# Kernel tuning notes

Measured on AMD Instinct MI355X. Metric: run time of the kernel, lower is better.

The kernel has to match this reference:

```python
import jax, jax.numpy as jnp
import numpy as np

N = 100000      # nodes
E = 1600000     # edges (before self-loops)
IN = 128        # in_channels
H = 8           # heads (layer 0)
C = 8           # hidden_node_channels_per_head
OUT = 64        # out_channels (layer 1, single head, concat=False)
NEG_SLOPE = 0.2 # PyG GATConv LeakyReLU slope


def setup_inputs() -> dict:
    key = jax.random.key(0)
    ks = jax.random.split(key, 10)
    x = jax.random.normal(ks[0], (N, IN), jnp.float32)
    edge_index = jax.random.randint(ks[1], (2, E), 0, N, dtype=jnp.int32)
    s0 = 1.0 / np.sqrt(IN)
    s1 = 1.0 / np.sqrt(H * C)
    return {
        "x": x,
        "edge_index": edge_index,
        "W0": jax.random.normal(ks[2], (IN, H * C), jnp.float32) * s0,
        "att_src0": jax.random.normal(ks[3], (H, C), jnp.float32) * s1,
        "att_dst0": jax.random.normal(ks[4], (H, C), jnp.float32) * s1,
        "b0": jnp.zeros((H * C,), jnp.float32),
        "W1": jax.random.normal(ks[5], (H * C, OUT), jnp.float32) * s1,
        "att_src1": jax.random.normal(ks[6], (1, OUT), jnp.float32) * s1,
        "att_dst1": jax.random.normal(ks[7], (1, OUT), jnp.float32) * s1,
        "b1": jnp.zeros((OUT,), jnp.float32),
    }


def _gat_conv(x, src, dst, W, a_src, a_dst, b, heads, ch, concat):
    # x: [N, F_in]; src/dst: [E'] (self-loops included)
    xW = (x @ W).reshape(N, heads, ch)                     # [N, H, C]
    a_s = jnp.einsum('nhc,hc->nh', xW, a_src)              # [N, H]
    a_d = jnp.einsum('nhc,hc->nh', xW, a_dst)              # [N, H]
    e = jax.nn.leaky_relu(a_s[src] + a_d[dst], NEG_SLOPE)  # [E', H]
    # segment softmax over incoming edges of each dst node
    m = jax.ops.segment_max(e, dst, num_segments=N)        # [N, H]
    ex = jnp.exp(e - m[dst])
    denom = jax.ops.segment_sum(ex, dst, num_segments=N)   # [N, H]
    alpha = ex / denom[dst]                                # [E', H]
    out = jax.ops.segment_sum(alpha[:, :, None] * xW[src], dst, num_segments=N)  # [N, H, C]
    if concat:
        return out.reshape(N, heads * ch) + b
    return out.mean(axis=1) + b


def reference(x, edge_index, W0, att_src0, att_dst0, b0, W1, att_src1, att_dst1, b1):
    src, dst = edge_index[0], edge_index[1]
    loops = jnp.arange(N, dtype=src.dtype)                 # PyG add_self_loops=True
    src = jnp.concatenate([src, loops])
    dst = jnp.concatenate([dst, loops])
    # layer 0: GATConv(IN -> C per head, H heads, concat) ; ELU (dropout = identity at eval)
    h = jax.nn.elu(_gat_conv(x, src, dst, W0, att_src0, att_dst0, b0, H, C, True))
    # layer 1: GATConv(H*C -> OUT, 1 head, concat=False) ; ELU
    out = jax.nn.elu(_gat_conv(h, src, dst, W1, att_src1, att_dst1, b1, 1, OUT, False))
    return out
```

## Files before the change

### kernel.cpp

```cpp
#include <hip/hip_runtime.h>
#include <hip/hip_fp16.h>
#include <math.h>


#define CAPS 12
#define STRIDE 12
#define NBMAX 512
#define SLOTS 6144
#define OVF   1024
#define REGION 7168
#define LOG2E 1.44269504f

typedef _Float16 h2_t  __attribute__((ext_vector_type(2)));
typedef _Float16 h8_t  __attribute__((ext_vector_type(8)));
typedef float    f4_t  __attribute__((ext_vector_type(4)));
typedef unsigned int u4_t __attribute__((ext_vector_type(4)));

__device__ __forceinline__ float lrelu(float v) { return v >= 0.f ? v : 0.2f * v; }
__device__ __forceinline__ float eluf(float v)  {
    return v > 0.f ? v : __builtin_amdgcn_exp2f(v * LOG2E) - 1.f;
}

#define MIX_LO(acc, pk, w) asm("v_fma_mix_f32 %0, %1, %2, %0 op_sel:[0,0,0] op_sel_hi:[1,0,0]" : "+v"(acc) : "v"(pk), "v"(w))
#define MIX_HI(acc, pk, w) asm("v_fma_mix_f32 %0, %1, %2, %0 op_sel:[1,0,0] op_sel_hi:[1,0,0]" : "+v"(acc) : "v"(pk), "v"(w))

__device__ __forceinline__ void gemm_body(
    int gb, const float* __restrict__ x, int N,
    __half* __restrict__ xw, float* __restrict__ as, float* __restrict__ ad,
    h8_t* Bl)
{
    int wave = threadIdx.x >> 6, lane = threadIdx.x & 63;
    int row0 = gb * 128 + wave * 16;
    if (row0 >= N) return;
    int quad = lane >> 4, c16 = lane & 15;
    int myrow = min(row0 + c16, N - 1);
    const float* xr = x + (size_t)myrow * 128;
    h8_t a[4];
    #pragma unroll
    for (int ks = 0; ks < 4; ks++) {
        int kb = ks * 32 + quad * 8;
        float4 v0 = *(const float4*)(xr + kb);
        float4 v1 = *(const float4*)(xr + kb + 4);
        h8_t av;
        av[0] = (_Float16)v0.x; av[1] = (_Float16)v0.y;
        av[2] = (_Float16)v0.z; av[3] = (_Float16)v0.w;
        av[4] = (_Float16)v1.x; av[5] = (_Float16)v1.y;
        av[6] = (_Float16)v1.z; av[7] = (_Float16)v1.w;
        a[ks] = av;
    }
    int rbase = row0 + quad * 4;
    #pragma unroll
    for (int ct = 0; ct < 5; ct++) {
        f4_t acc = {0.f, 0.f, 0.f, 0.f};
        #pragma unroll
        for (int ks = 0; ks < 4; ks++) {
            h8_t b = Bl[(ct * 4 + ks) * 64 + lane];
            acc = __builtin_amdgcn_mfma_f32_16x16x32_f16(a[ks], b, acc, 0, 0, 0);
        }
        if (ct < 4) {
            int col = ct * 16 + c16;
            #pragma unroll
            for (int r = 0; r < 4; r++) {
                int row = rbase + r;
                if (row < N) xw[(size_t)row * 64 + col] = __float2half(acc[r]);
            }
        } else {
            #pragma unroll
            for (int r = 0; r < 4; r++) {
                int row = rbase + r;
                if (row < N) {
                    float sc = acc[r] * LOG2E;
                    if (c16 < 8) as[(size_t)row * 8 + c16] = sc;
                    else         ad[(size_t)row * 8 + (c16 - 8)] = sc;
                }
            }
        }
    }
}

__global__ __launch_bounds__(512, 4) void kGB(
    const float* __restrict__ x, const float* __restrict__ W0,
    const float* __restrict__ aS0, const float* __restrict__ aD0, int N,
    __half* __restrict__ xw, float* __restrict__ as, float* __restrict__ ad,
    int gemmBlocks,
    const int* __restrict__ src, const int* __restrict__ dst, int E, int perBlock,
    unsigned* __restrict__ bucketBuf, int* __restrict__ gcur, int* __restrict__ cntT,
    int NB, int binBlocks)
{
    __shared__ __align__(16) char smem[NBMAX * STRIDE * 4 + NBMAX * 4];
    int b = blockIdx.x;
    int T = gemmBlocks + binBlocks;
    int lo = (int)((long long)b * gemmBlocks / T);
    int hi = (int)((long long)(b + 1) * gemmBlocks / T);
    if (hi > lo) {
        h8_t* Bl = (h8_t*)smem;
        for (int g = threadIdx.x; g < 1280; g += 512) {
            int col  = g & 15;
            int quad = (g >> 4) & 3;
            int ks   = (g >> 6) & 3;
            int ct   = g >> 8;
            h8_t av;
            if (ct < 4) {
                #pragma unroll
                for (int j = 0; j < 8; j++) {
                    int k = ks * 32 + quad * 8 + j;
                    av[j] = (_Float16)W0[k * 64 + ct * 16 + col];
                }
            } else {
                int h = col & 7;
                const float* att = (col < 8) ? aS0 : aD0;
                #pragma unroll
                for (int j = 0; j < 8; j++) {
                    int k = ks * 32 + quad * 8 + j;
                    float v = 0.f;
                    #pragma unroll
                    for (int cc = 0; cc < 8; cc++)
                        v += W0[k * 64 + h * 8 + cc] * att[h * 8 + cc];
                    av[j] = (_Float16)v;
                }
            }
            Bl[g] = av;
        }
        __syncthreads();
        gemm_body(lo, x, N, xw, as, ad, Bl);
    } else {
        int pb = b - hi;
        unsigned* stage = (unsigned*)smem;
        int* scnt = (int*)(smem + NBMAX * STRIDE * 4);
        int tid = threadIdx.x;
        for (int i = tid; i < NB; i += 512) scnt[i] = 0;
        __syncthreads();
        int e0 = pb * perBlock, e1 = min(E, e0 + perBlock);
        for (int i = e0 + tid; i < e1; i += 512) {
            int d2 = dst[i], s2 = src[i];
            int bk = d2 >> 8;
            unsigned rec = ((unsigned)(d2 & 255) << 22) | (unsigned)s2;
            int pos = atomicAdd(&scnt[bk], 1);
            if (pos < CAPS) {
                stage[bk * STRIDE + pos] = rec;
            } else {
                int g = atomicAdd(&gcur[bk], 1);
                if (g < OVF) bucketBuf[(size_t)bk * REGION + SLOTS + g] = rec;
            }
        }
        __syncthreads();
        const uint4* stv = (const uint4*)stage;
        for (int t = tid; t < NB; t += 512) {
            int n = min(scnt[t], CAPS);
            cntT[(size_t)pb * NBMAX + t] = n;
            uint4* gp = (uint4*)&bucketBuf[(size_t)t * REGION + (size_t)pb * CAPS];
            gp[0] = stv[t * 3 + 0];
            gp[1] = stv[t * 3 + 1];
            gp[2] = stv[t * 3 + 2];
        }
    }
}

__global__ __launch_bounds__(256) void kP2(
    const unsigned* __restrict__ bucketBuf, const int* __restrict__ gcur,
    const int* __restrict__ cntT, int NB, int N,
    int* __restrict__ rowS, int* __restrict__ rowE, int* __restrict__ adj)
{
    __shared__ int cnts[512];
    __shared__ int deg[256];
    __shared__ int curl[256];
    __shared__ int sc[256];
    int b = blockIdx.x, tid = threadIdx.x;
    int lo = b << 8;
    int hi = min(N, lo + 256);
    int cnt = hi - lo;
    for (int i = tid; i < 512; i += 256) cnts[i] = cntT[(size_t)i * NBMAX + b];
    deg[tid] = 0;
    __syncthreads();
    const unsigned* buf = bucketBuf + (size_t)b * REGION;
    for (int blk = tid; blk < 512; blk += 256) {
        int c = cnts[blk];
        const unsigned* p = buf + blk * CAPS;
        for (int i2 = 0; i2 < c; i2++) atomicAdd(&deg[p[i2] >> 22], 1);
    }
    int ovf = min(gcur[b], OVF);
    for (int e = tid; e < ovf; e += 256) atomicAdd(&deg[buf[SLOTS + e] >> 22], 1);
    __syncthreads();
    int d = deg[tid];
    sc[tid] = d;
    __syncthreads();
    for (int off2 = 1; off2 < 256; off2 <<= 1) {
        int xv = (tid >= off2) ? sc[tid - off2] : 0;
        __syncthreads();
        sc[tid] += xv;
        __syncthreads();
    }
    int base = b * REGION;
    int o = (tid ? sc[tid - 1] : 0);
    curl[tid] = base + o;
    if (tid < cnt) { rowS[lo + tid] = base + o; rowE[lo + tid] = base + o + d; }
    __syncthreads();
    for (int blk = tid; blk < 512; blk += 256) {
        int c = cnts[blk];
        const unsigned* p = buf + blk * CAPS;
        for (int i2 = 0; i2 < c; i2++) {
            unsigned r = p[i2];
            int pp = atomicAdd(&curl[r >> 22], 1);
            adj[pp] = (int)(r & 0x3FFFFF);
        }
    }
    for (int e = tid; e < ovf; e += 256) {
        unsigned r = buf[SLOTS + e];
        int pp = atomicAdd(&curl[r >> 22], 1);
        adj[pp] = (int)(r & 0x3FFFFF);
    }
}

__global__ __launch_bounds__(512) void k_agg8(
    const __half* __restrict__ xw, const float* __restrict__ as, const float* __restrict__ ad,
    const int* __restrict__ rowS, const int* __restrict__ rowE, const int* __restrict__ adj,
    const float* __restrict__ bias,
    const float* __restrict__ W1, const float* __restrict__ aS1, const float* __restrict__ aD1,
    int N, __half* __restrict__ hw, float* __restrict__ as1, float* __restrict__ ad1)
{
    __shared__ __align__(16) h8_t Wl[512];
    __shared__ __align__(16) h8_t hst[32][9];
    {
        int g = threadIdx.x;
        int col  = g & 15;
        int quad = (g >> 4) & 3;
        int ks   = (g >> 6) & 1;
        int ct   = g >> 7;
        h8_t av;
        #pragma unroll
        for (int j = 0; j < 8; j++) {
            int k = ks * 32 + quad * 8 + j;
            av[j] = (_Float16)W1[k * 64 + ct * 16 + col];
        }
        Wl[g] = av;
    }
    int n = (blockIdx.x * 512 + threadIdx.x) >> 4;
    int sub  = threadIdx.x & 15;
    bool active = n < N;
    int e2 = sub >> 3;
    int hh = sub & 7;
    int rs = active ? rowS[n] : 0;
    int re = active ? rowE[n] : 0;
    const u4_t* xwv = (const u4_t*)xw;
    unsigned nc = active ? (unsigned)n : 0u;
    float adv = ad[nc * 8u + hh];
    float shift = lrelu(as[nc * 8u + hh] + adv);
    float accv[8];
    #pragma unroll
    for (int k = 0; k < 8; k++) accv[k] = 0.f;
    float dsum = 0.f;

    int j = rs;
    bool vA0 = j + e2 < re,     vB0 = j + 2 + e2 < re;
    int  sA0 = adj[(unsigned)(vA0 ? j + e2 : 0)];
    int  sB0 = adj[(unsigned)(vB0 ? j + 2 + e2 : 0)];
    bool vA1 = j + 4 + e2 < re, vB1 = j + 6 + e2 < re;
    int  sA1 = adj[(unsigned)(vA1 ? j + 4 + e2 : 0)];
    int  sB1 = adj[(unsigned)(vB1 ? j + 6 + e2 : 0)];
    float eA0 = lrelu(as[(unsigned)sA0 * 8u + hh] + adv);
    float eB0 = lrelu(as[(unsigned)sB0 * 8u + hh] + adv);
    u4_t xA0 = xwv[(unsigned)sA0 * 8u + hh];
    u4_t xB0 = xwv[(unsigned)sB0 * 8u + hh];
    float eA1, eB1; u4_t xA1, xB1;

    for (;;) {
        {
            bool vA2 = j + 8 + e2 < re, vB2 = j + 10 + e2 < re;
            int nsA = adj[(unsigned)(vA2 ? j + 8 + e2 : 0)];
            int nsB = adj[(unsigned)(vB2 ? j + 10 + e2 : 0)];
            eA1 = lrelu(as[(unsigned)sA1 * 8u + hh] + adv);
            eB1 = lrelu(as[(unsigned)sB1 * 8u + hh] + adv);
            xA1 = xwv[(unsigned)sA1 * 8u + hh];
            xB1 = xwv[(unsigned)sB1 * 8u + hh];
            float wA = vA0 ? __builtin_amdgcn_exp2f(eA0 - shift) : 0.f;
            float wB = vB0 ? __builtin_amdgcn_exp2f(eB0 - shift) : 0.f;
            dsum += wA + wB;
            #pragma unroll
            for (int q = 0; q < 4; q++) {
                MIX_LO(accv[2 * q],     xA0[q], wA);
                MIX_HI(accv[2 * q + 1], xA0[q], wA);
            }
            #pragma unroll
            for (int q = 0; q < 4; q++) {
                MIX_LO(accv[2 * q],     xB0[q], wB);
                MIX_HI(accv[2 * q + 1], xB0[q], wB);
            }
            vA0 = vA2; vB0 = vB2; sA0 = nsA; sB0 = nsB;
        }
        j += 4;
        if (!__any(vA1)) break;
        {
            bool vA2 = j + 8 + e2 < re, vB2 = j + 10 + e2 < re;
            int nsA = adj[(unsigned)(vA2 ? j + 8 + e2 : 0)];
            int nsB = adj[(unsigned)(vB2 ? j + 10 + e2 : 0)];
            eA0 = lrelu(as[(unsigned)sA0 * 8u + hh] + adv);
            eB0 = lrelu(as[(unsigned)sB0 * 8u + hh] + adv);
            xA0 = xwv[(unsigned)sA0 * 8u + hh];
            xB0 = xwv[(unsigned)sB0 * 8u + hh];
            float wA = vA1 ? __builtin_amdgcn_exp2f(eA1 - shift) : 0.f;
            float wB = vB1 ? __builtin_amdgcn_exp2f(eB1 - shift) : 0.f;
            dsum += wA + wB;
            #pragma unroll
            for (int q = 0; q < 4; q++) {
                MIX_LO(accv[2 * q],     xA1[q], wA);
                MIX_HI(accv[2 * q + 1], xA1[q], wA);
            }
            #pragma unroll
            for (int q = 0; q < 4; q++) {
                MIX_LO(accv[2 * q],     xB1[q], wB);
                MIX_HI(accv[2 * q + 1], xB1[q], wB);
            }
            vA1 = vA2; vB1 = vB2; sA1 = nsA; sB1 = nsB;
        }
        j += 4;
        if (!__any(vA0)) break;
    }
    #pragma unroll
    for (int k = 0; k < 8; k++) accv[k] += __shfl_xor(accv[k], 8, 64);
    dsum += __shfl_xor(dsum, 8, 64);
    if (e2 == 0) {
        int nl = (threadIdx.x >> 4);
        h8_t o;
        if (active) {
            float inv = 1.f / (1.f + dsum);
            h8_t sv = *(const h8_t*)(xw + (size_t)n * 64 + hh * 8);
            float4 b0 = *(const float4*)(bias + hh * 8);
            float4 b1 = *(const float4*)(bias + hh * 8 + 4);
            float bb[8] = {b0.x, b0.y, b0.z, b0.w, b1.x, b1.y, b1.z, b1.w};
            #pragma unroll
            for (int k = 0; k < 8; k++) {
                float v = (accv[k] + (float)sv[k]) * inv + bb[k];
                o[k] = (_Float16)eluf(v);
            }
        } else {
            #pragma unroll
            for (int k = 0; k < 8; k++) o[k] = (_Float16)0.f;
        }
        hst[nl][hh] = o;
    }
    __syncthreads();
    int wave = threadIdx.x >> 6, lane = threadIdx.x & 63;
    if (wave < 2) {
        int quad = lane >> 4, c16 = lane & 15;
        int lrow = wave * 16 + c16;
        int row0 = blockIdx.x * 32 + wave * 16;
        h8_t a0 = hst[lrow][quad];
        h8_t a1 = hst[lrow][4 + quad];
        int rbase = row0 + quad * 4;
        float ps[4] = {0.f, 0.f, 0.f, 0.f};
        float pd[4] = {0.f, 0.f, 0.f, 0.f};
        #pragma unroll
        for (int ct = 0; ct < 4; ct++) {
            f4_t acc = {0.f, 0.f, 0.f, 0.f};
            acc = __builtin_amdgcn_mfma_f32_16x16x32_f16(a0, Wl[(ct * 2 + 0) * 64 + lane], acc, 0, 0, 0);
            acc = __builtin_amdgcn_mfma_f32_16x16x32_f16(a1, Wl[(ct * 2 + 1) * 64 + lane], acc, 0, 0, 0);
            float s1c = aS1[ct * 16 + c16];
            float d1c = aD1[ct * 16 + c16];
            int col = ct * 16 + c16;
            #pragma unroll
            for (int r = 0; r < 4; r++) {
                int rr = rbase + r;
                if (rr < N) hw[(size_t)rr * 64 + col] = __float2half(acc[r]);
                ps[r] = fmaf(acc[r], s1c, ps[r]);
                pd[r] = fmaf(acc[r], d1c, pd[r]);
            }
        }
        #pragma unroll
        for (int r = 0; r < 4; r++) {
            #pragma unroll
            for (int off = 1; off < 16; off <<= 1) {
                ps[r] += __shfl_xor(ps[r], off, 64);
                pd[r] += __shfl_xor(pd[r], off, 64);
            }
        }
        if (c16 == 0) {
            #pragma unroll
            for (int r = 0; r < 4; r++) {
                int rr = rbase + r;
                if (rr < N) { as1[rr] = ps[r] * LOG2E; ad1[rr] = pd[r] * LOG2E; }
            }
        }
    }
}

__global__ __launch_bounds__(512) void k_agg1(
    const __half* __restrict__ hw, const float* __restrict__ as, const float* __restrict__ ad,
    const int* __restrict__ rowS, const int* __restrict__ rowE, const int* __restrict__ adj,
    const float* __restrict__ bias, int N, float* __restrict__ outp)
{
    int n = (blockIdx.x * 512 + threadIdx.x) >> 4;
    int sub  = threadIdx.x & 15;
    if (n >= N) return;
    int e2 = sub >> 3;
    int hh = sub & 7;
    int rs = rowS[n], re = rowE[n];
    const u4_t* hwv = (const u4_t*)hw;
    float adv = ad[n];
    float shift = lrelu(as[n] + adv);
    float accv[8];
    #pragma unroll
    for (int k = 0; k < 8; k++) accv[k] = 0.f;
    float dsum = 0.f;

    int j = rs;
    bool vA0 = j + e2 < re,     vB0 = j + 2 + e2 < re;
    int  sA0 = adj[(unsigned)(vA0 ? j + e2 : 0)];
    int  sB0 = adj[(unsigned)(vB0 ? j + 2 + e2 : 0)];
    bool vA1 = j + 4 + e2 < re, vB1 = j + 6 + e2 < re;
    int  sA1 = adj[(unsigned)(vA1 ? j + 4 + e2 : 0)];
    int  sB1 = adj[(unsigned)(vB1 ? j + 6 + e2 : 0)];
    float eA0 = lrelu(as[(unsigned)sA0] + adv);
    float eB0 = lrelu(as[(unsigned)sB0] + adv);
    u4_t xA0 = hwv[(unsigned)sA0 * 8u + hh];
    u4_t xB0 = hwv[(unsigned)sB0 * 8u + hh];
    float eA1, eB1; u4_t xA1, xB1;

    for (;;) {
        {
            bool vA2 = j + 8 + e2 < re, vB2 = j + 10 + e2 < re;
            int nsA = adj[(unsigned)(vA2 ? j + 8 + e2 : 0)];
            int nsB = adj[(unsigned)(vB2 ? j + 10 + e2 : 0)];
            eA1 = lrelu(as[(unsigned)sA1] + adv);
            eB1 = lrelu(as[(unsigned)sB1] + adv);
            xA1 = hwv[(unsigned)sA1 * 8u + hh];
            xB1 = hwv[(unsigned)sB1 * 8u + hh];
            float wA = vA0 ? __builtin_amdgcn_exp2f(eA0 - shift) : 0.f;
            float wB = vB0 ? __builtin_amdgcn_exp2f(eB0 - shift) : 0.f;
            dsum += wA + wB;
            #pragma unroll
            for (int q = 0; q < 4; q++) {
                MIX_LO(accv[2 * q],     xA0[q], wA);
                MIX_HI(accv[2 * q + 1], xA0[q], wA);
            }
            #pragma unroll
            for (int q = 0; q < 4; q++) {
                MIX_LO(accv[2 * q],     xB0[q], wB);
                MIX_HI(accv[2 * q + 1], xB0[q], wB);
            }
            vA0 = vA2; vB0 = vB2; sA0 = nsA; sB0 = nsB;
        }
        j += 4;
        if (!__any(vA1)) break;
        {
            bool vA2 = j + 8 + e2 < re, vB2 = j + 10 + e2 < re;
            int nsA = adj[(unsigned)(vA2 ? j + 8 + e2 : 0)];
            int nsB = adj[(unsigned)(vB2 ? j + 10 + e2 : 0)];
            eA0 = lrelu(as[(unsigned)sA0] + adv);
            eB0 = lrelu(as[(unsigned)sB0] + adv);
            xA0 = hwv[(unsigned)sA0 * 8u + hh];
            xB0 = hwv[(unsigned)sB0 * 8u + hh];
            float wA = vA1 ? __builtin_amdgcn_exp2f(eA1 - shift) : 0.f;
            float wB = vB1 ? __builtin_amdgcn_exp2f(eB1 - shift) : 0.f;
            dsum += wA + wB;
            #pragma unroll
            for (int q = 0; q < 4; q++) {
                MIX_LO(accv[2 * q],     xA1[q], wA);
                MIX_HI(accv[2 * q + 1], xA1[q], wA);
            }
            #pragma unroll
            for (int q = 0; q < 4; q++) {
                MIX_LO(accv[2 * q],     xB1[q], wB);
                MIX_HI(accv[2 * q + 1], xB1[q], wB);
            }
            vA1 = vA2; vB1 = vB2; sA1 = nsA; sB1 = nsB;
        }
        j += 4;
        if (!__any(vA0)) break;
    }
    #pragma unroll
    for (int k = 0; k < 8; k++) accv[k] += __shfl_xor(accv[k], 8, 64);
    dsum += __shfl_xor(dsum, 8, 64);
    if (e2 == 0) {
        float inv = 1.f / (1.f + dsum);
        h8_t sv = *(const h8_t*)(hw + (size_t)n * 64 + hh * 8);
        float4 b0 = *(const float4*)(bias + hh * 8);
        float4 b1 = *(const float4*)(bias + hh * 8 + 4);
        float bb[8] = {b0.x, b0.y, b0.z, b0.w, b1.x, b1.y, b1.z, b1.w};
        float ov[8];
        #pragma unroll
        for (int k = 0; k < 8; k++)
            ov[k] = eluf((accv[k] + (float)sv[k]) * inv + bb[k]);
        float4 o0 = {ov[0], ov[1], ov[2], ov[3]};
        float4 o1 = {ov[4], ov[5], ov[6], ov[7]};
        float4* op = (float4*)(outp + (size_t)n * 64 + hh * 8);
        op[0] = o0;
        op[1] = o1;
    }
}

extern "C" void kernel_launch(void* const* d_in, const int* in_sizes, int n_in,
                              void* d_out, int out_size, void* d_ws, size_t ws_size,
                              hipStream_t stream)
{
    const float* x   = (const float*)d_in[0];
    const int*   ei  = (const int*)d_in[1];
    const float* W0  = (const float*)d_in[2];
    const float* aS0 = (const float*)d_in[3];
    const float* aD0 = (const float*)d_in[4];
    const float* b0  = (const float*)d_in[5];
    const float* W1  = (const float*)d_in[6];
    const float* aS1 = (const float*)d_in[7];
    const float* aD1 = (const float*)d_in[8];
    const float* b1  = (const float*)d_in[9];

    const int N = in_sizes[0] / 128;
    const int E = in_sizes[1] / 2;
    const int* srcp = ei;
    const int* dstp = ei + E;

    const int NB  = (N + 255) >> 8;

    char* ws = (char*)d_ws;
    size_t off = 0;
    auto alloc = [&](size_t bytes) -> size_t {
        size_t o = off;
        off = (o + bytes + 255) & ~(size_t)255;
        return o;
    };
    __half* B1 = (__half*)(ws + alloc((size_t)N * 64 * 2));
    size_t b2Bytes = (size_t)N * 64 * 2;
    size_t bkBytes = (size_t)NB * REGION * 4;
    char*  region  = ws + alloc(b2Bytes > bkBytes ? b2Bytes : bkBytes);
    __half*   B2        = (__half*)region;
    unsigned* bucketBuf = (unsigned*)region;
    float* as0 = (float*)(ws + alloc((size_t)N * 8 * 4));
    float* ad0 = (float*)(ws + alloc((size_t)N * 8 * 4));
    float* as1 = (float*)(ws + alloc((size_t)N * 4));
    float* ad1 = (float*)(ws + alloc((size_t)N * 4));
    int*  rowS = (int*)(ws + alloc((size_t)(N + 1) * 4));
    int*  rowE = (int*)(ws + alloc((size_t)(N + 1) * 4));
    int*   adj = (int*)(ws + alloc((size_t)NB * REGION * 4));
    int*  gcur = (int*)(ws + alloc((size_t)NB * 4));
    int*  cntT = (int*)(ws + alloc((size_t)NBMAX * NBMAX * 4));

    const int gemmBlocks = (N + 127) / 128;
    const int binBlocks  = 512;
    const int perBlock   = (E + binBlocks - 1) / binBlocks;

    hipMemsetAsync(gcur, 0, (size_t)NB * 4, stream);
    kGB<<<gemmBlocks + binBlocks, 512, 0, stream>>>(
        x, W0, aS0, aD0, N, B1, as0, ad0, gemmBlocks,
        srcp, dstp, E, perBlock, bucketBuf, gcur, cntT, NB, binBlocks);
    kP2<<<NB, 256, 0, stream>>>(bucketBuf, gcur, cntT, NB, N, rowS, rowE, adj);

    const int agBlocks = (N + 31) / 32;
    k_agg8<<<agBlocks, 512, 0, stream>>>(B1, as0, ad0, rowS, rowE, adj, b0,
                                         W1, aS1, aD1, N, B2, as1, ad1);
    k_agg1<<<agBlocks, 512, 0, stream>>>(B2, as1, ad1, rowS, rowE, adj, b1, N, (float*)d_out);
}
```

Baseline: 238.5 us.

## Store layer-0 attention scores in fp16 and spread layer-1 GEMM across all waves

Layer-0 per-node attention logits (as0/ad0) are now written and gathered as fp16 instead of fp32, halving the bytes of the random per-edge gathers in the aggregation kernel. The fused layer-1 projection epilogue in k_agg8 is redistributed so all 8 waves each compute one column tile of one row half, instead of 2 waves looping over 4 column tiles. Partial attention dot products are then combined through shared memory with an extra barrier. The fp16 logits lower precision of the softmax inputs, and the epilogue change adds a sync and LDS traffic.

```diff
diff --git a/kernel.cpp b/kernel.cpp
--- a/kernel.cpp
+++ b/kernel.cpp
@@ -26,7 +26,7 @@
 
 __device__ __forceinline__ void gemm_body(
     int gb, const float* __restrict__ x, int N,
-    __half* __restrict__ xw, float* __restrict__ as, float* __restrict__ ad,
+    __half* __restrict__ xw, __half* __restrict__ as, __half* __restrict__ ad,
     h8_t* Bl)
 {
     int wave = threadIdx.x >> 6, lane = threadIdx.x & 63;
@@ -70,8 +70,8 @@
                 int row = rbase + r;
                 if (row < N) {
                     float sc = acc[r] * LOG2E;
-                    if (c16 < 8) as[(size_t)row * 8 + c16] = sc;
-                    else         ad[(size_t)row * 8 + (c16 - 8)] = sc;
+                    if (c16 < 8) as[(size_t)row * 8 + c16] = __float2half(sc);
+                    else         ad[(size_t)row * 8 + (c16 - 8)] = __float2half(sc);
                 }
             }
         }
@@ -81,7 +81,7 @@
 __global__ __launch_bounds__(512, 4) void kGB(
     const float* __restrict__ x, const float* __restrict__ W0,
     const float* __restrict__ aS0, const float* __restrict__ aD0, int N,
-    __half* __restrict__ xw, float* __restrict__ as, float* __restrict__ ad,
+    __half* __restrict__ xw, __half* __restrict__ as, __half* __restrict__ ad,
     int gemmBlocks,
     const int* __restrict__ src, const int* __restrict__ dst, int E, int perBlock,
     unsigned* __restrict__ bucketBuf, int* __restrict__ gcur, int* __restrict__ cntT,
@@ -212,7 +212,7 @@
 }
 
 __global__ __launch_bounds__(512) void k_agg8(
-    const __half* __restrict__ xw, const float* __restrict__ as, const float* __restrict__ ad,
+    const __half* __restrict__ xw, const __half* __restrict__ as, const __half* __restrict__ ad,
     const int* __restrict__ rowS, const int* __restrict__ rowE, const int* __restrict__ adj,
     const float* __restrict__ bias,
     const float* __restrict__ W1, const float* __restrict__ aS1, const float* __restrict__ aD1,
@@ -220,6 +220,8 @@
 {
     __shared__ __align__(16) h8_t Wl[512];
     __shared__ __align__(16) h8_t hst[32][9];
+    __shared__ float psum[4][32];
+    __shared__ float pdsum[4][32];
     {
         int g = threadIdx.x;
         int col  = g & 15;
@@ -243,8 +245,8 @@
     int re = active ? rowE[n] : 0;
     const u4_t* xwv = (const u4_t*)xw;
     unsigned nc = active ? (unsigned)n : 0u;
-    float adv = ad[nc * 8u + hh];
-    float shift = lrelu(as[nc * 8u + hh] + adv);
+    float adv = __half2float(ad[nc * 8u + hh]);
+    float shift = lrelu(__half2float(as[nc * 8u + hh]) + adv);
     float accv[8];
     #pragma unroll
     for (int k = 0; k < 8; k++) accv[k] = 0.f;
@@ -257,8 +259,8 @@
     bool vA1 = j + 4 + e2 < re, vB1 = j + 6 + e2 < re;
     int  sA1 = adj[(unsigned)(vA1 ? j + 4 + e2 : 0)];
     int  sB1 = adj[(unsigned)(vB1 ? j + 6 + e2 : 0)];
-    float eA0 = lrelu(as[(unsigned)sA0 * 8u + hh] + adv);
-    float eB0 = lrelu(as[(unsigned)sB0 * 8u + hh] + adv);
+    float eA0 = lrelu(__half2float(as[(unsigned)sA0 * 8u + hh]) + adv);
+    float eB0 = lrelu(__half2float(as[(unsigned)sB0 * 8u + hh]) + adv);
     u4_t xA0 = xwv[(unsigned)sA0 * 8u + hh];
     u4_t xB0 = xwv[(unsigned)sB0 * 8u + hh];
     float eA1, eB1; u4_t xA1, xB1;
@@ -268,8 +270,8 @@
             bool vA2 = j + 8 + e2 < re, vB2 = j + 10 + e2 < re;
             int nsA = adj[(unsigned)(vA2 ? j + 8 + e2 : 0)];
             int nsB = adj[(unsigned)(vB2 ? j + 10 + e2 : 0)];
-            eA1 = lrelu(as[(unsigned)sA1 * 8u + hh] + adv);
-            eB1 = lrelu(as[(unsigned)sB1 * 8u + hh] + adv);
+            eA1 = lrelu(__half2float(as[(unsigned)sA1 * 8u + hh]) + adv);
+            eB1 = lrelu(__half2float(as[(unsigned)sB1 * 8u + hh]) + adv);
             xA1 = xwv[(unsigned)sA1 * 8u + hh];
             xB1 = xwv[(unsigned)sB1 * 8u + hh];
             float wA = vA0 ? __builtin_amdgcn_exp2f(eA0 - shift) : 0.f;
@@ -293,8 +295,8 @@
             bool vA2 = j + 8 + e2 < re, vB2 = j + 10 + e2 < re;
             int nsA = adj[(unsigned)(vA2 ? j + 8 + e2 : 0)];
             int nsB = adj[(unsigned)(vB2 ? j + 10 + e2 : 0)];
-            eA0 = lrelu(as[(unsigned)sA0 * 8u + hh] + adv);
-            eB0 = lrelu(as[(unsigned)sB0 * 8u + hh] + adv);
+            eA0 = lrelu(__half2float(as[(unsigned)sA0 * 8u + hh]) + adv);
+            eB0 = lrelu(__half2float(as[(unsigned)sB0 * 8u + hh]) + adv);
             xA0 = xwv[(unsigned)sA0 * 8u + hh];
             xB0 = xwv[(unsigned)sB0 * 8u + hh];
             float wA = vA1 ? __builtin_amdgcn_exp2f(eA1 - shift) : 0.f;
@@ -339,31 +341,29 @@
         hst[nl][hh] = o;
     }
     __syncthreads();
-    int wave = threadIdx.x >> 6, lane = threadIdx.x & 63;
-    if (wave < 2) {
+    {
+        int wave = threadIdx.x >> 6, lane = threadIdx.x & 63;
+        int ct   = wave >> 1;
+        int half = wave & 1;
         int quad = lane >> 4, c16 = lane & 15;
-        int lrow = wave * 16 + c16;
-        int row0 = blockIdx.x * 32 + wave * 16;
+        int lrow = half * 16 + c16;
+        int row0 = blockIdx.x * 32 + half * 16;
         h8_t a0 = hst[lrow][quad];
         h8_t a1 = hst[lrow][4 + quad];
         int rbase = row0 + quad * 4;
-        float ps[4] = {0.f, 0.f, 0.f, 0.f};
-        float pd[4] = {0.f, 0.f, 0.f, 0.f};
+        f4_t acc = {0.f, 0.f, 0.f, 0.f};
+        acc = __builtin_amdgcn_mfma_f32_16x16x32_f16(a0, Wl[(ct * 2 + 0) * 64 + lane], acc, 0, 0, 0);
+        acc = __builtin_amdgcn_mfma_f32_16x16x32_f16(a1, Wl[(ct * 2 + 1) * 64 + lane], acc, 0, 0, 0);
+        float s1c = aS1[ct * 16 + c16];
+        float d1c = aD1[ct * 16 + c16];
+        int col = ct * 16 + c16;
+        float ps[4], pd[4];
         #pragma unroll
-        for (int ct = 0; ct < 4; ct++) {
-            f4_t acc = {0.f, 0.f, 0.f, 0.f};
-            acc = __builtin_amdgcn_mfma_f32_16x16x32_f16(a0, Wl[(ct * 2 + 0) * 64 + lane], acc, 0, 0, 0);
-            acc = __builtin_amdgcn_mfma_f32_16x16x32_f16(a1, Wl[(ct * 2 + 1) * 64 + lane], acc, 0, 0, 0);
-            float s1c = aS1[ct * 16 + c16];
-            float d1c = aD1[ct * 16 + c16];
-            int col = ct * 16 + c16;
-            #pragma unroll
-            for (int r = 0; r < 4; r++) {
-                int rr = rbase + r;
-                if (rr < N) hw[(size_t)rr * 64 + col] = __float2half(acc[r]);
-                ps[r] = fmaf(acc[r], s1c, ps[r]);
-                pd[r] = fmaf(acc[r], d1c, pd[r]);
-            }
+        for (int r = 0; r < 4; r++) {
+            int rr = rbase + r;
+            if (rr < N) hw[(size_t)rr * 64 + col] = __float2half(acc[r]);
+            ps[r] = acc[r] * s1c;
+            pd[r] = acc[r] * d1c;
         }
         #pragma unroll
         for (int r = 0; r < 4; r++) {
@@ -376,9 +376,21 @@
         if (c16 == 0) {
             #pragma unroll
             for (int r = 0; r < 4; r++) {
-                int rr = rbase + r;
-                if (rr < N) { as1[rr] = ps[r] * LOG2E; ad1[rr] = pd[r] * LOG2E; }
-            }
+                int lr = half * 16 + quad * 4 + r;
+                psum[ct][lr]  = ps[r];
+                pdsum[ct][lr] = pd[r];
+            }
+        }
+    }
+    __syncthreads();
+    if (threadIdx.x < 32) {
+        int lr = threadIdx.x;
+        int rr = blockIdx.x * 32 + lr;
+        if (rr < N) {
+            float s  = psum[0][lr] + psum[1][lr] + psum[2][lr] + psum[3][lr];
+            float dd = pdsum[0][lr] + pdsum[1][lr] + pdsum[2][lr] + pdsum[3][lr];
+            as1[rr] = s * LOG2E;
+            ad1[rr] = dd * LOG2E;
         }
     }
 }
@@ -523,8 +535,8 @@
     char*  region  = ws + alloc(b2Bytes > bkBytes ? b2Bytes : bkBytes);
     __half*   B2        = (__half*)region;
     unsigned* bucketBuf = (unsigned*)region;
-    float* as0 = (float*)(ws + alloc((size_t)N * 8 * 4));
-    float* ad0 = (float*)(ws + alloc((size_t)N * 8 * 4));
+    __half* as0 = (__half*)(ws + alloc((size_t)N * 8 * 2));
+    __half* ad0 = (__half*)(ws + alloc((size_t)N * 8 * 2));
     float* as1 = (float*)(ws + alloc((size_t)N * 4));
     float* ad1 = (float*)(ws + alloc((size_t)N * 4));
     int*  rowS = (int*)(ws + alloc((size_t)(N + 1) * 4));
```

After: 232.1 us. 1.03x faster.
